# Performance work log

Hardware: AMD Instinct MI355X
Metric: run time of the kernel (lower is better)

## Reference

```python
import jax, jax.numpy as jnp
import numpy as np

N = 50000      # nodes
E = 800000     # edges
H = 128        # hidden_features
DEPTH = 5
G = 64         # graphs in batch
EPS = 1e-5


def _ln(x, g, b):
    m = jnp.mean(x, axis=-1, keepdims=True)
    v = jnp.mean((x - m) ** 2, axis=-1, keepdims=True)
    return (x - m) * jax.lax.rsqrt(v + EPS) * g + b


def _lin_init(key, fan_in, fan_out):
    s = 1.0 / np.sqrt(fan_in)
    kw, kb = jax.random.split(key)
    return (jax.random.uniform(kw, (fan_in, fan_out), jnp.float32, -s, s),
            jax.random.uniform(kb, (fan_out,), jnp.float32, -s, s))


def setup_inputs() -> dict:
    key = jax.random.key(0)
    ks = jax.random.split(key, 16)
    inp = {
        'x': jax.random.normal(ks[0], (N, 1), jnp.float32),
        'pos': jax.random.normal(ks[1], (N, 3), jnp.float32),
        'edge_index': jax.random.randint(ks[2], (2, E), 0, N, jnp.int32),
        'cell_offset': jax.random.normal(ks[3], (E, 3), jnp.float32),
        'unit_cell': jax.random.normal(ks[4], (3, 3), jnp.float32),
        'batch_ids': jnp.sort(jax.random.randint(ks[5], (N,), 0, G, jnp.int32)),
    }
    inp['emb_w'], inp['emb_b'] = _lin_init(ks[6], 1, H)
    # stacked per-layer params for lax.scan
    def stack(fn):
        outs = [fn(jax.random.fold_in(ks[7], i)) for i in range(DEPTH)]
        return tuple(jnp.stack(t) for t in zip(*outs))
    def layer_params(k):
        k1, k2, k3, k4 = jax.random.split(k, 4)
        mw1, mb1 = _lin_init(k1, 2 * H + 1, H)
        mw2, mb2 = _lin_init(k2, H, H)
        uw1, ub1 = _lin_init(k3, 2 * H, H)
        uw2, ub2 = _lin_init(k4, H, H)
        ones = jnp.ones((H,), jnp.float32); zeros = jnp.zeros((H,), jnp.float32)
        return (mw1, mb1, ones, zeros, mw2, mb2, ones, zeros,
                uw1, ub1, ones, zeros, uw2, ub2, ones, zeros)
    (inp['msg_w1'], inp['msg_b1'], inp['msg_g1'], inp['msg_be1'],
     inp['msg_w2'], inp['msg_b2'], inp['msg_g2'], inp['msg_be2'],
     inp['upd_w1'], inp['upd_b1'], inp['upd_g1'], inp['upd_be1'],
     inp['upd_w2'], inp['upd_b2'], inp['upd_g2'], inp['upd_be2']) = stack(layer_params)
    inp['pred_w1'], inp['pred_b1'] = _lin_init(ks[8], H, H)
    inp['pred_w2'], inp['pred_b2'] = _lin_init(ks[9], H, 1)
    return inp


def reference(x, pos, edge_index, cell_offset, unit_cell, batch_ids,
              emb_w, emb_b,
              msg_w1, msg_b1, msg_g1, msg_be1, msg_w2, msg_b2, msg_g2, msg_be2,
              upd_w1, upd_b1, upd_g1, upd_be1, upd_w2, upd_b2, upd_g2, upd_be2,
              pred_w1, pred_b1, pred_w2, pred_b2):
    src, dst = edge_index[0], edge_index[1]  # PyG: x_j = source, x_i = target
    h = x @ emb_w + emb_b  # [N, H]
    # PBC distances
    corrected = pos[dst] - cell_offset @ unit_cell  # [E, 3]
    dist = jnp.linalg.norm(corrected - pos[src], axis=-1, keepdims=True)  # [E, 1]

    def step(h, p):
        (mw1, mb1, mg1, mbe1, mw2, mb2, mg2, mbe2,
         uw1, ub1, ug1, ube1, uw2, ub2, ug2, ube2) = p
        msg = jnp.concatenate([h[dst], h[src], dist], axis=-1)  # [E, 2H+1]
        msg = jax.nn.relu(_ln(msg @ mw1 + mb1, mg1, mbe1))
        msg = jax.nn.relu(_ln(msg @ mw2 + mb2, mg2, mbe2))
        aggr = jax.ops.segment_sum(msg, dst, num_segments=N)  # scatter-add to targets
        u = jnp.concatenate([h, aggr], axis=-1)  # [N, 2H]
        u = jax.nn.relu(_ln(u @ uw1 + ub1, ug1, ube1))
        u = jax.nn.relu(_ln(u @ uw2 + ub2, ug2, ube2))
        return h + u, None  # residual

    params = (msg_w1, msg_b1, msg_g1, msg_be1, msg_w2, msg_b2, msg_g2, msg_be2,
              upd_w1, upd_b1, upd_g1, upd_be1, upd_w2, upd_b2, upd_g2, upd_be2)
    h, _ = jax.lax.scan(step, h, params)
    pooled = jax.ops.segment_sum(h, batch_ids, num_segments=G)  # global_add_pool
    return jax.nn.relu(pooled @ pred_w1 + pred_b1) @ pred_w2 + pred_b2  # [G, 1]
```

## Files before the change

kernel.cpp:

```cpp
#include <hip/hip_runtime.h>
#include <hip/hip_bf16.h>

#define NN 50000
#define NE 800000
#define HD 128
#define DEPTH 5
#define NG 64
#define LNEPS 1e-5f

typedef __attribute__((ext_vector_type(8))) short bf8;
typedef __attribute__((ext_vector_type(4))) float f4;

static __device__ __forceinline__ unsigned short bf1(float x) {
    __hip_bfloat16 b = __float2bfloat16(x);
    unsigned short r;
    __builtin_memcpy(&r, &b, 2);
    return r;
}
static __device__ __forceinline__ unsigned int cvt2(float a, float b) {
    float2 t; t.x = a; t.y = b;
    __hip_bfloat162 h = __float22bfloat162_rn(t);
    unsigned int r;
    __builtin_memcpy(&r, &h, 4);
    return r;
}

__global__ void pack_weights(const float* __restrict__ msg_w1, const float* __restrict__ msg_w2,
                             const float* __restrict__ upd_w1, const float* __restrict__ upd_w2,
                             unsigned short* __restrict__ packed) {
    const int which = blockIdx.y & 3, layer = blockIdx.y >> 2;
    const int t = blockIdx.x * 256 + threadIdx.x;
    const float* src; int K; unsigned short* dst;
    unsigned short* lbase = packed + layer * 98304;
    if (which == 0)      { src = msg_w1 + layer*257*HD; K = 256; dst = lbase; }
    else if (which == 1) { src = msg_w2 + layer*HD*HD;  K = 128; dst = lbase + 32768; }
    else if (which == 2) { src = upd_w1 + layer*256*HD; K = 256; dst = lbase + 49152; }
    else                 { src = upd_w2 + layer*HD*HD;  K = 128; dst = lbase + 81920; }
    if (t >= K * HD) return;
    const int e = t & 7, l = (t >> 3) & 63, f = (t >> 9) & 7, s = t >> 12;
    const int kk = s*32 + ((l >> 4) << 3) + e;
    const int k = (which & 1) ? ((kk & 7)*16 + (kk >> 3)) : kk;
    const int n = f*16 + (l & 15);
    dst[t] = bf1(src[k*HD + n]);
}

__global__ void embed_kernel(const float* __restrict__ x, const float* __restrict__ emb_w,
                             const float* __restrict__ emb_b,
                             float* __restrict__ h, unsigned short* __restrict__ hb) {
    const int i = blockIdx.x * 256 + threadIdx.x;
    const int n = i >> 7, j = i & 127;
    const float v = x[n] * emb_w[j] + emb_b[j];
    h[i] = v; hb[i] = bf1(v);
}

__global__ void hist_kernel(const int* __restrict__ ei, int* __restrict__ cnt) {
    const int e = blockIdx.x * 256 + threadIdx.x;
    atomicAdd(&cnt[ei[NE + e]], 1);
}

__global__ __launch_bounds__(1024) void scan_kernel(const int* __restrict__ cnt,
                                                    int* __restrict__ cur) {
    __shared__ int part[1024];
    const int t = threadIdx.x;
    const int per = 49;
    const int base = t * per;
    int s = 0;
    for (int i = 0; i < per; ++i) { const int idx = base + i; if (idx < NN) s += cnt[idx]; }
    part[t] = s; __syncthreads();
    for (int st = 1; st < 1024; st <<= 1) {
        const int v = (t >= st) ? part[t - st] : 0;
        __syncthreads();
        part[t] += v;
        __syncthreads();
    }
    int run = (t == 0) ? 0 : part[t - 1];
    for (int i = 0; i < per; ++i) {
        const int idx = base + i;
        if (idx < NN) { cur[idx] = run; run += cnt[idx]; }
    }
}

__global__ void scatter_kernel(const int* __restrict__ ei, int* __restrict__ cur,
                               int* __restrict__ sidx, int* __restrict__ ssrc,
                               int* __restrict__ sdst) {
    const int e = blockIdx.x * 256 + threadIdx.x;
    const int d = ei[NE + e];
    const int p = atomicAdd(&cur[d], 1);
    sidx[p] = e; ssrc[p] = ei[e]; sdst[p] = d;
}

__global__ void dist_kernel(const float* __restrict__ pos, const int* __restrict__ sidx,
                            const int* __restrict__ ssrc, const int* __restrict__ sdst,
                            const float* __restrict__ cell, const float* __restrict__ U,
                            float* __restrict__ dist) {
    const int p = blockIdx.x * 256 + threadIdx.x;
    const int e = sidx[p];
    const int s = ssrc[p], d = sdst[p];
    const float c0 = cell[e*3], c1 = cell[e*3+1], c2 = cell[e*3+2];
    const float ox = c0*U[0] + c1*U[3] + c2*U[6];
    const float oy = c0*U[1] + c1*U[4] + c2*U[7];
    const float oz = c0*U[2] + c1*U[5] + c2*U[8];
    const float dx = pos[d*3]   - ox - pos[s*3];
    const float dy = pos[d*3+1] - oy - pos[s*3+1];
    const float dz = pos[d*3+2] - oz - pos[s*3+2];
    dist[p] = sqrtf(dx*dx + dy*dy + dz*dz);
}

__global__ __launch_bounds__(128, 4) void edge_kernel(
    const unsigned short* __restrict__ hb, const float* __restrict__ dist,
    const int* __restrict__ ssrc, const int* __restrict__ sdst,
    const unsigned short* __restrict__ pw,
    const float* __restrict__ w1last, const float* __restrict__ b1,
    const float* __restrict__ g1, const float* __restrict__ be1,
    const float* __restrict__ b2, const float* __restrict__ g2,
    const float* __restrict__ be2, float* __restrict__ aggr)
{
    __shared__ unsigned short lds[64 * 128];
    __shared__ int dstl[64];
    char* ldsb = (char*)lds;
    const int tid = threadIdx.x, blk = blockIdx.x;
    const int l = tid & 63, wv = tid >> 6;
    const int li = l & 15, gq = l >> 4;

    if (tid < 64) dstl[tid] = sdst[blk*64 + tid];

    const int rowA = wv*32 + li, rowB = rowA + 16;
    const int eA = blk*64 + rowA, eB = blk*64 + rowB;
    const unsigned short* pDA = hb + sdst[eA]*HD + gq*8;
    const unsigned short* pSA = hb + ssrc[eA]*HD + gq*8;
    const unsigned short* pDB = hb + sdst[eB]*HD + gq*8;
    const unsigned short* pSB = hb + ssrc[eB]*HD + gq*8;

    f4 acc[2][8];
    #pragma unroll
    for (int m = 0; m < 2; ++m)
        #pragma unroll
        for (int f = 0; f < 8; ++f) { f4 z = {0.f,0.f,0.f,0.f}; acc[m][f] = z; }

    #pragma unroll
    for (int s = 0; s < 8; ++s) {
        bf8 breg[8];
        #pragma unroll
        for (int f = 0; f < 8; ++f) breg[f] = *(const bf8*)(pw + s*4096 + f*512 + l*8);
        const bf8 aA = (s < 4) ? *(const bf8*)(pDA + s*32) : *(const bf8*)(pSA + (s-4)*32);
        const bf8 aB = (s < 4) ? *(const bf8*)(pDB + s*32) : *(const bf8*)(pSB + (s-4)*32);
        #pragma unroll
        for (int f = 0; f < 8; ++f) {
            acc[0][f] = __builtin_amdgcn_mfma_f32_16x16x32_bf16(aA, breg[f], acc[0][f], 0, 0, 0);
            acc[1][f] = __builtin_amdgcn_mfma_f32_16x16x32_bf16(aB, breg[f], acc[1][f], 0, 0, 0);
        }
    }

    {
        float bb[8], wl[8], gg[8], be[8];
        #pragma unroll
        for (int f = 0; f < 8; ++f) {
            const int n = f*16 + li;
            bb[f] = b1[n]; wl[f] = w1last[n]; gg[f] = g1[n]; be[f] = be1[n];
        }
        #pragma unroll
        for (int m = 0; m < 2; ++m) {
            const float4 d4 = *(const float4*)(dist + blk*64 + wv*32 + m*16 + gq*4);
            const float dsv[4] = {d4.x, d4.y, d4.z, d4.w};
            float ps[4] = {0,0,0,0}, pq[4] = {0,0,0,0};
            #pragma unroll
            for (int f = 0; f < 8; ++f)
                #pragma unroll
                for (int r = 0; r < 4; ++r) {
                    const float v = acc[m][f][r] + bb[f] + dsv[r]*wl[f];
                    acc[m][f][r] = v;
                    ps[r] += v; pq[r] += v*v;
                }
            #pragma unroll
            for (int mm = 1; mm < 16; mm <<= 1)
                #pragma unroll
                for (int r = 0; r < 4; ++r) {
                    ps[r] += __shfl_xor(ps[r], mm);
                    pq[r] += __shfl_xor(pq[r], mm);
                }
            #pragma unroll
            for (int r = 0; r < 4; ++r) {
                const float mean = ps[r] * (1.f/HD);
                const float rstd = rsqrtf(pq[r]*(1.f/HD) - mean*mean + LNEPS);
                const int row = wv*32 + m*16 + gq*4 + r;
                float vv[8];
                #pragma unroll
                for (int f = 0; f < 8; ++f)
                    vv[f] = fmaxf((acc[m][f][r] - mean)*rstd*gg[f] + be[f], 0.f);
                uint4 u;
                u.x = cvt2(vv[0], vv[1]); u.y = cvt2(vv[2], vv[3]);
                u.z = cvt2(vv[4], vv[5]); u.w = cvt2(vv[6], vv[7]);
                *(uint4*)(ldsb + ((row*256 + li*16) ^ ((row & 7) << 4))) = u;
            }
        }
    }

    const unsigned short* pw2 = pw + 32768;
    f4 acc2[2][8];
    #pragma unroll
    for (int m = 0; m < 2; ++m)
        #pragma unroll
        for (int f = 0; f < 8; ++f) { f4 z = {0.f,0.f,0.f,0.f}; acc2[m][f] = z; }
    #pragma unroll
    for (int s = 0; s < 4; ++s) {
        bf8 breg[8];
        #pragma unroll
        for (int f = 0; f < 8; ++f) breg[f] = *(const bf8*)(pw2 + s*4096 + f*512 + l*8);
        #pragma unroll
        for (int m = 0; m < 2; ++m) {
            const int ar = wv*32 + m*16 + li;
            const bf8 a = *(const bf8*)(ldsb + ((ar*256 + s*64 + gq*16) ^ ((ar & 7) << 4)));
            #pragma unroll
            for (int f = 0; f < 8; ++f)
                acc2[m][f] = __builtin_amdgcn_mfma_f32_16x16x32_bf16(a, breg[f], acc2[m][f], 0, 0, 0);
        }
    }

    {
        float bb2[8], gg2[8], be2v[8];
        #pragma unroll
        for (int f = 0; f < 8; ++f) {
            const int n = f*16 + li;
            bb2[f] = b2[n]; gg2[f] = g2[n]; be2v[f] = be2[n];
        }
        #pragma unroll
        for (int m = 0; m < 2; ++m) {
            float ps[4] = {0,0,0,0}, pq[4] = {0,0,0,0};
            #pragma unroll
            for (int f = 0; f < 8; ++f)
                #pragma unroll
                for (int r = 0; r < 4; ++r) {
                    const float v = acc2[m][f][r] + bb2[f];
                    acc2[m][f][r] = v;
                    ps[r] += v; pq[r] += v*v;
                }
            #pragma unroll
            for (int mm = 1; mm < 16; mm <<= 1)
                #pragma unroll
                for (int r = 0; r < 4; ++r) {
                    ps[r] += __shfl_xor(ps[r], mm);
                    pq[r] += __shfl_xor(pq[r], mm);
                }
            #pragma unroll
            for (int r = 0; r < 4; ++r) {
                const float mean = ps[r] * (1.f/HD);
                const float rstd = rsqrtf(pq[r]*(1.f/HD) - mean*mean + LNEPS);
                const int row = wv*32 + m*16 + gq*4 + r;
                float vv[8];
                #pragma unroll
                for (int f = 0; f < 8; ++f)
                    vv[f] = fmaxf((acc2[m][f][r] - mean)*rstd*gg2[f] + be2v[f], 0.f);
                uint4 u;
                u.x = cvt2(vv[0], vv[1]); u.y = cvt2(vv[2], vv[3]);
                u.z = cvt2(vv[4], vv[5]); u.w = cvt2(vv[6], vv[7]);
                *(uint4*)(ldsb + ((row*256 + li*16) ^ ((row & 7) << 4))) = u;
            }
        }
    }
    __syncthreads();

    {
        const int j = tid;
        const int jj = (j & 7)*16 + (j >> 3);
        int curd = dstl[0];
        float a0 = 0.f;
        #pragma unroll 4
        for (int row = 0; row < 64; ++row) {
            const int d = dstl[row];
            const unsigned short u = *(const unsigned short*)(ldsb + ((row*256 + j*2) ^ ((row & 7) << 4)));
            const float v = __uint_as_float(((unsigned int)u) << 16);
            if (d != curd) { unsafeAtomicAdd(&aggr[curd*HD + jj], a0); a0 = 0.f; curd = d; }
            a0 += v;
        }
        unsafeAtomicAdd(&aggr[curd*HD + jj], a0);
    }
}

__global__ __launch_bounds__(128, 4) void node_kernel(
    unsigned short* __restrict__ hb, float* __restrict__ aggr,
    const unsigned short* __restrict__ pw,
    const float* __restrict__ b1, const float* __restrict__ g1, const float* __restrict__ be1,
    const float* __restrict__ b2, const float* __restrict__ g2, const float* __restrict__ be2,
    float* __restrict__ h)
{
    __shared__ unsigned short lds[64 * 128];
    char* ldsb = (char*)lds;
    const int tid = threadIdx.x, blk = blockIdx.x;
    const int l = tid & 63, wv = tid >> 6;
    const int li = l & 15, gq = l >> 4;

    const int rowA = wv*32 + li, rowB = rowA + 16;
    const int nA = blk*64 + rowA, nB = blk*64 + rowB;
    const int ncA = (nA < NN) ? nA : NN - 1;
    const int ncB = (nB < NN) ? nB : NN - 1;
    const unsigned short* pHA = hb + ncA*HD + gq*8;
    const unsigned short* pHB = hb + ncB*HD + gq*8;
    float* pAA = aggr + ncA*HD + gq*8;
    float* pAB = aggr + ncB*HD + gq*8;

    f4 acc[2][8];
    #pragma unroll
    for (int m = 0; m < 2; ++m)
        #pragma unroll
        for (int f = 0; f < 8; ++f) { f4 z = {0.f,0.f,0.f,0.f}; acc[m][f] = z; }

    #pragma unroll
    for (int s = 0; s < 8; ++s) {
        bf8 breg[8];
        #pragma unroll
        for (int f = 0; f < 8; ++f) breg[f] = *(const bf8*)(pw + s*4096 + f*512 + l*8);
        bf8 aA, aB;
        if (s < 4) {
            aA = *(const bf8*)(pHA + s*32);
            aB = *(const bf8*)(pHB + s*32);
        } else {
            const float4 a0 = *(const float4*)(pAA + (s-4)*32);
            const float4 a1 = *(const float4*)(pAA + (s-4)*32 + 4);
            const float4 c0 = *(const float4*)(pAB + (s-4)*32);
            const float4 c1 = *(const float4*)(pAB + (s-4)*32 + 4);
            union { unsigned int u[4]; bf8 v; } pk;
            pk.u[0] = cvt2(a0.x, a0.y); pk.u[1] = cvt2(a0.z, a0.w);
            pk.u[2] = cvt2(a1.x, a1.y); pk.u[3] = cvt2(a1.z, a1.w);
            aA = pk.v;
            pk.u[0] = cvt2(c0.x, c0.y); pk.u[1] = cvt2(c0.z, c0.w);
            pk.u[2] = cvt2(c1.x, c1.y); pk.u[3] = cvt2(c1.z, c1.w);
            aB = pk.v;
        }
        #pragma unroll
        for (int f = 0; f < 8; ++f) {
            acc[0][f] = __builtin_amdgcn_mfma_f32_16x16x32_bf16(aA, breg[f], acc[0][f], 0, 0, 0);
            acc[1][f] = __builtin_amdgcn_mfma_f32_16x16x32_bf16(aB, breg[f], acc[1][f], 0, 0, 0);
        }
    }

    {
        const float4 z = {0.f,0.f,0.f,0.f};
        #pragma unroll
        for (int s = 0; s < 4; ++s) {
            if (nA < NN) { *(float4*)(pAA + s*32) = z; *(float4*)(pAA + s*32 + 4) = z; }
            if (nB < NN) { *(float4*)(pAB + s*32) = z; *(float4*)(pAB + s*32 + 4) = z; }
        }
    }

    {
        float bb[8], gg[8], be[8];
        #pragma unroll
        for (int f = 0; f < 8; ++f) {
            const int n = f*16 + li;
            bb[f] = b1[n]; gg[f] = g1[n]; be[f] = be1[n];
        }
        #pragma unroll
        for (int m = 0; m < 2; ++m) {
            float ps[4] = {0,0,0,0}, pq[4] = {0,0,0,0};
            #pragma unroll
            for (int f = 0; f < 8; ++f)
                #pragma unroll
                for (int r = 0; r < 4; ++r) {
                    const float v = acc[m][f][r] + bb[f];
                    acc[m][f][r] = v;
                    ps[r] += v; pq[r] += v*v;
                }
            #pragma unroll
            for (int mm = 1; mm < 16; mm <<= 1)
                #pragma unroll
                for (int r = 0; r < 4; ++r) {
                    ps[r] += __shfl_xor(ps[r], mm);
                    pq[r] += __shfl_xor(pq[r], mm);
                }
            #pragma unroll
            for (int r = 0; r < 4; ++r) {
                const float mean = ps[r] * (1.f/HD);
                const float rstd = rsqrtf(pq[r]*(1.f/HD) - mean*mean + LNEPS);
                const int row = wv*32 + m*16 + gq*4 + r;
                float vv[8];
                #pragma unroll
                for (int f = 0; f < 8; ++f)
                    vv[f] = fmaxf((acc[m][f][r] - mean)*rstd*gg[f] + be[f], 0.f);
                uint4 u;
                u.x = cvt2(vv[0], vv[1]); u.y = cvt2(vv[2], vv[3]);
                u.z = cvt2(vv[4], vv[5]); u.w = cvt2(vv[6], vv[7]);
                *(uint4*)(ldsb + ((row*256 + li*16) ^ ((row & 7) << 4))) = u;
            }
        }
    }

    const unsigned short* pw2 = pw + 32768;
    f4 acc2[2][8];
    #pragma unroll
    for (int m = 0; m < 2; ++m)
        #pragma unroll
        for (int f = 0; f < 8; ++f) { f4 z = {0.f,0.f,0.f,0.f}; acc2[m][f] = z; }
    #pragma unroll
    for (int s = 0; s < 4; ++s) {
        bf8 breg[8];
        #pragma unroll
        for (int f = 0; f < 8; ++f) breg[f] = *(const bf8*)(pw2 + s*4096 + f*512 + l*8);
        #pragma unroll
        for (int m = 0; m < 2; ++m) {
            const int ar = wv*32 + m*16 + li;
            const bf8 a = *(const bf8*)(ldsb + ((ar*256 + s*64 + gq*16) ^ ((ar & 7) << 4)));
            #pragma unroll
            for (int f = 0; f < 8; ++f)
                acc2[m][f] = __builtin_amdgcn_mfma_f32_16x16x32_bf16(a, breg[f], acc2[m][f], 0, 0, 0);
        }
    }

    {
        float bb2[8], gg2[8], be2v[8];
        #pragma unroll
        for (int f = 0; f < 8; ++f) {
            const int n = f*16 + li;
            bb2[f] = b2[n]; gg2[f] = g2[n]; be2v[f] = be2[n];
        }
        #pragma unroll
        for (int m = 0; m < 2; ++m) {
            float ps[4] = {0,0,0,0}, pq[4] = {0,0,0,0};
            #pragma unroll
            for (int f = 0; f < 8; ++f)
                #pragma unroll
                for (int r = 0; r < 4; ++r) {
                    const float v = acc2[m][f][r] + bb2[f];
                    acc2[m][f][r] = v;
                    ps[r] += v; pq[r] += v*v;
                }
            #pragma unroll
            for (int mm = 1; mm < 16; mm <<= 1)
                #pragma unroll
                for (int r = 0; r < 4; ++r) {
                    ps[r] += __shfl_xor(ps[r], mm);
                    pq[r] += __shfl_xor(pq[r], mm);
                }
            #pragma unroll
            for (int r = 0; r < 4; ++r) {
                const int node = blk*64 + wv*32 + m*16 + gq*4 + r;
                if (node < NN) {
                    const float mean = ps[r] * (1.f/HD);
                    const float rstd = rsqrtf(pq[r]*(1.f/HD) - mean*mean + LNEPS);
                    #pragma unroll
                    for (int f = 0; f < 8; ++f) {
                        const int n = f*16 + li;
                        float v = (acc2[m][f][r] - mean)*rstd*gg2[f] + be2v[f];
                        v = fmaxf(v, 0.f);
                        const int idx = node*HD + n;
                        const float nh = h[idx] + v;
                        h[idx] = nh;
                        hb[idx] = bf1(nh);
                    }
                }
            }
        }
    }
}

__global__ void pool_kernel(const float* __restrict__ h, const int* __restrict__ bids,
                            float* __restrict__ pooled) {
    const int j = threadIdx.x;
    const int n0 = blockIdx.x * 256;
    if (n0 >= NN) return;
    int cur = bids[n0];
    float acc = 0.f;
    for (int i = 0; i < 256; ++i) {
        const int n = n0 + i;
        if (n >= NN) break;
        const int b = bids[n];
        if (b != cur) { unsafeAtomicAdd(&pooled[cur*HD + j], acc); acc = 0.f; cur = b; }
        acc += h[n*HD + j];
    }
    unsafeAtomicAdd(&pooled[cur*HD + j], acc);
}

__global__ void pred_kernel(const float* __restrict__ pooled, const float* __restrict__ w1,
                            const float* __restrict__ pb1, const float* __restrict__ w2,
                            const float* __restrict__ pb2, float* __restrict__ out) {
    const int g = blockIdx.x, j = threadIdx.x;
    __shared__ float pg[128];
    __shared__ float red[128];
    pg[j] = pooled[g*HD + j];
    __syncthreads();
    float z = pb1[j];
    for (int k = 0; k < 128; ++k) z += pg[k] * w1[k*HD + j];
    red[j] = fmaxf(z, 0.f) * w2[j];
    __syncthreads();
    for (int st = 64; st > 0; st >>= 1) {
        if (j < st) red[j] += red[j + st];
        __syncthreads();
    }
    if (j == 0) out[g] = red[0] + pb2[0];
}

extern "C" void kernel_launch(void* const* d_in, const int* in_sizes, int n_in,
                              void* d_out, int out_size, void* d_ws, size_t ws_size,
                              hipStream_t stream) {
    const float* x       = (const float*)d_in[0];
    const float* pos     = (const float*)d_in[1];
    const int*   ei      = (const int*)  d_in[2];
    const float* cell    = (const float*)d_in[3];
    const float* U       = (const float*)d_in[4];
    const int*   bids    = (const int*)  d_in[5];
    const float* emb_w   = (const float*)d_in[6];
    const float* emb_b   = (const float*)d_in[7];
    const float* msg_w1  = (const float*)d_in[8];
    const float* msg_b1  = (const float*)d_in[9];
    const float* msg_g1  = (const float*)d_in[10];
    const float* msg_be1 = (const float*)d_in[11];
    const float* msg_w2  = (const float*)d_in[12];
    const float* msg_b2  = (const float*)d_in[13];
    const float* msg_g2  = (const float*)d_in[14];
    const float* msg_be2 = (const float*)d_in[15];
    const float* upd_w1  = (const float*)d_in[16];
    const float* upd_b1  = (const float*)d_in[17];
    const float* upd_g1  = (const float*)d_in[18];
    const float* upd_be1 = (const float*)d_in[19];
    const float* upd_w2  = (const float*)d_in[20];
    const float* upd_b2  = (const float*)d_in[21];
    const float* upd_g2  = (const float*)d_in[22];
    const float* upd_be2 = (const float*)d_in[23];
    const float* pred_w1 = (const float*)d_in[24];
    const float* pred_b1 = (const float*)d_in[25];
    const float* pred_w2 = (const float*)d_in[26];
    const float* pred_b2 = (const float*)d_in[27];

    char* ws = (char*)d_ws;
    float*          h      = (float*)          ws;
    unsigned short* hb     = (unsigned short*)(ws + 25600000);
    float*          aggr   = (float*)         (ws + 38400000);
    float*          dist   = (float*)         (ws + 64000000);
    float*          pooled = (float*)         (ws + 67200000);
    unsigned short* packed = (unsigned short*)(ws + 67232768);
    int*            cnt    = (int*)           (ws + 68215808);
    int*            cur    = (int*)           (ws + 68416512);
    int*            sidx   = (int*)           (ws + 68617216);
    int*            ssrc   = (int*)           (ws + 71817216);
    int*            sdst   = (int*)           (ws + 75017216);

    hipMemsetAsync(aggr, 0, (size_t)NN * HD * sizeof(float), stream);
    hipMemsetAsync(pooled, 0, (size_t)NG * HD * sizeof(float), stream);
    hipMemsetAsync(cnt, 0, (size_t)NN * sizeof(int), stream);

    dim3 pgrid(128, DEPTH * 4);
    pack_weights<<<pgrid, 256, 0, stream>>>(msg_w1, msg_w2, upd_w1, upd_w2, packed);
    embed_kernel<<<(NN * HD) / 256, 256, 0, stream>>>(x, emb_w, emb_b, h, hb);

    hist_kernel<<<NE / 256, 256, 0, stream>>>(ei, cnt);
    scan_kernel<<<1, 1024, 0, stream>>>(cnt, cur);
    scatter_kernel<<<NE / 256, 256, 0, stream>>>(ei, cur, sidx, ssrc, sdst);
    dist_kernel<<<NE / 256, 256, 0, stream>>>(pos, sidx, ssrc, sdst, cell, U, dist);

    for (int layer = 0; layer < DEPTH; ++layer) {
        const unsigned short* pl = packed + layer * 98304;
        edge_kernel<<<NE / 64, 128, 0, stream>>>(
            hb, dist, ssrc, sdst, pl,
            msg_w1 + layer*257*HD + 256*HD,
            msg_b1 + layer*HD, msg_g1 + layer*HD, msg_be1 + layer*HD,
            msg_b2 + layer*HD, msg_g2 + layer*HD, msg_be2 + layer*HD,
            aggr);
        node_kernel<<<(NN + 63) / 64, 128, 0, stream>>>(
            hb, aggr, pl + 49152,
            upd_b1 + layer*HD, upd_g1 + layer*HD, upd_be1 + layer*HD,
            upd_b2 + layer*HD, upd_g2 + layer*HD, upd_be2 + layer*HD,
            h);
    }

    pool_kernel<<<(NN + 255) / 256, 128, 0, stream>>>(h, bids, pooled);
    pred_kernel<<<NG, 128, 0, stream>>>(pooled, pred_w1, pred_b1, pred_w2, pred_b2, (float*)d_out);
}
```

Baseline: 1.414 ms.

## Precompute per-node first message-layer projections and gather them per edge

The first message linear layer is split by linearity: h@W_dst (plus bias) and h@W_src are computed once per node in a new y_kernel. The edge kernel then gathers and adds the two projected rows plus the distance term instead of running a K=256 MFMA GEMM per edge. This cuts the first-layer GEMM work from per-edge to per-node, at the cost of an extra kernel, a 256-wide bf16 y buffer, and an extra bf16 rounding of the pre-LayerNorm sums. Per-edge gathers stay the same size (two 128-wide bf16 rows).

```diff
diff --git a/kernel.cpp b/kernel.cpp
--- a/kernel.cpp
+++ b/kernel.cpp
@@ -25,15 +25,25 @@
     return r;
 }
 
+
 __global__ void pack_weights(const float* __restrict__ msg_w1, const float* __restrict__ msg_w2,
                              const float* __restrict__ upd_w1, const float* __restrict__ upd_w2,
                              unsigned short* __restrict__ packed) {
     const int which = blockIdx.y & 3, layer = blockIdx.y >> 2;
     const int t = blockIdx.x * 256 + threadIdx.x;
+    unsigned short* lbase = packed + layer * 98304;
+    if (which == 0) {
+        if (t >= 32768) return;
+        const int e = t & 7, l = (t >> 3) & 63, f = (t >> 9) & 15, s = t >> 13;
+        const int k = s*32 + ((l >> 4) << 3) + e;
+        const float* W = msg_w1 + layer*257*HD;
+        const float v = (f < 8) ? W[k*HD + f*16 + (l & 15)]
+                                : W[(k + 128)*HD + (f - 8)*16 + (l & 15)];
+        lbase[t] = bf1(v);
+        return;
+    }
     const float* src; int K; unsigned short* dst;
-    unsigned short* lbase = packed + layer * 98304;
-    if (which == 0)      { src = msg_w1 + layer*257*HD; K = 256; dst = lbase; }
-    else if (which == 1) { src = msg_w2 + layer*HD*HD;  K = 128; dst = lbase + 32768; }
+    if (which == 1)      { src = msg_w2 + layer*HD*HD;  K = 128; dst = lbase + 32768; }
     else if (which == 2) { src = upd_w1 + layer*256*HD; K = 256; dst = lbase + 49152; }
     else                 { src = upd_w2 + layer*HD*HD;  K = 128; dst = lbase + 81920; }
     if (t >= K * HD) return;
@@ -42,6 +52,19 @@
     const int k = (which & 1) ? ((kk & 7)*16 + (kk >> 3)) : kk;
     const int n = f*16 + (l & 15);
     dst[t] = bf1(src[k*HD + n]);
+}
+
+__global__ void pack_sig(const float* __restrict__ msg_w1, const float* __restrict__ msg_g1,
+                         const float* __restrict__ msg_be1, float* __restrict__ sig) {
+    const int t = blockIdx.x * 256 + threadIdx.x;
+    if (t >= DEPTH * 384) return;
+    const int layer = t / 384, w3 = (t % 384) / 128, i = t % 128;
+    const int col = (i & 7)*16 + (i >> 3);
+    float v;
+    if (w3 == 0)      v = msg_w1[layer*257*HD + 256*HD + col];
+    else if (w3 == 1) v = msg_g1[layer*HD + col];
+    else              v = msg_be1[layer*HD + col];
+    sig[t] = v;
 }
 
 __global__ void embed_kernel(const float* __restrict__ x, const float* __restrict__ emb_w,
@@ -106,12 +129,67 @@
     dist[p] = sqrtf(dx*dx + dy*dy + dz*dz);
 }
 
+__global__ void y_kernel(const unsigned short* __restrict__ hb,
+                         const unsigned short* __restrict__ pw,
+                         const float* __restrict__ b1, unsigned short* __restrict__ y) {
+    const int tid = threadIdx.x, blk = blockIdx.x;
+    const int l = tid & 63, wv = tid >> 6;
+    const int li = l & 15, gq = l >> 4;
+    const int rowA = wv*32 + li, rowB = rowA + 16;
+    const int nA = blk*64 + rowA, nB = blk*64 + rowB;
+    const int ncA = (nA < NN) ? nA : NN - 1;
+    const int ncB = (nB < NN) ? nB : NN - 1;
+    const unsigned short* pHA = hb + ncA*HD + gq*8;
+    const unsigned short* pHB = hb + ncB*HD + gq*8;
+
+    f4 acc[2][16];
+    #pragma unroll
+    for (int m = 0; m < 2; ++m)
+        #pragma unroll
+        for (int f = 0; f < 16; ++f) { f4 z = {0.f,0.f,0.f,0.f}; acc[m][f] = z; }
+
+    #pragma unroll
+    for (int s = 0; s < 4; ++s) {
+        const bf8 aA = *(const bf8*)(pHA + s*32);
+        const bf8 aB = *(const bf8*)(pHB + s*32);
+        #pragma unroll
+        for (int f = 0; f < 16; ++f) {
+            const bf8 b = *(const bf8*)(pw + s*8192 + f*512 + l*8);
+            acc[0][f] = __builtin_amdgcn_mfma_f32_16x16x32_bf16(aA, b, acc[0][f], 0, 0, 0);
+            acc[1][f] = __builtin_amdgcn_mfma_f32_16x16x32_bf16(aB, b, acc[1][f], 0, 0, 0);
+        }
+    }
+
+    float bv[8];
+    #pragma unroll
+    for (int f = 0; f < 8; ++f) bv[f] = b1[f*16 + li];
+
+    #pragma unroll
+    for (int m = 0; m < 2; ++m)
+        #pragma unroll
+        for (int r = 0; r < 4; ++r) {
+            const int node = blk*64 + wv*32 + m*16 + gq*4 + r;
+            if (node < NN) {
+                uint4 u;
+                u.x = cvt2(acc[m][0][r]+bv[0], acc[m][1][r]+bv[1]);
+                u.y = cvt2(acc[m][2][r]+bv[2], acc[m][3][r]+bv[3]);
+                u.z = cvt2(acc[m][4][r]+bv[4], acc[m][5][r]+bv[5]);
+                u.w = cvt2(acc[m][6][r]+bv[6], acc[m][7][r]+bv[7]);
+                *(uint4*)(y + node*256 + li*8) = u;
+                uint4 v;
+                v.x = cvt2(acc[m][8][r],  acc[m][9][r]);
+                v.y = cvt2(acc[m][10][r], acc[m][11][r]);
+                v.z = cvt2(acc[m][12][r], acc[m][13][r]);
+                v.w = cvt2(acc[m][14][r], acc[m][15][r]);
+                *(uint4*)(y + node*256 + 128 + li*8) = v;
+            }
+        }
+}
+
 __global__ __launch_bounds__(128, 4) void edge_kernel(
-    const unsigned short* __restrict__ hb, const float* __restrict__ dist,
+    const unsigned short* __restrict__ y, const float* __restrict__ dist,
     const int* __restrict__ ssrc, const int* __restrict__ sdst,
-    const unsigned short* __restrict__ pw,
-    const float* __restrict__ w1last, const float* __restrict__ b1,
-    const float* __restrict__ g1, const float* __restrict__ be1,
+    const unsigned short* __restrict__ pw2, const float* __restrict__ sig,
     const float* __restrict__ b2, const float* __restrict__ g2,
     const float* __restrict__ be2, float* __restrict__ aggr)
 {
@@ -124,78 +202,67 @@
 
     if (tid < 64) dstl[tid] = sdst[blk*64 + tid];
 
-    const int rowA = wv*32 + li, rowB = rowA + 16;
-    const int eA = blk*64 + rowA, eB = blk*64 + rowB;
-    const unsigned short* pDA = hb + sdst[eA]*HD + gq*8;
-    const unsigned short* pSA = hb + ssrc[eA]*HD + gq*8;
-    const unsigned short* pDB = hb + sdst[eB]*HD + gq*8;
-    const unsigned short* pSB = hb + ssrc[eB]*HD + gq*8;
-
-    f4 acc[2][8];
-    #pragma unroll
-    for (int m = 0; m < 2; ++m)
-        #pragma unroll
-        for (int f = 0; f < 8; ++f) { f4 z = {0.f,0.f,0.f,0.f}; acc[m][f] = z; }
-
-    #pragma unroll
-    for (int s = 0; s < 8; ++s) {
-        bf8 breg[8];
-        #pragma unroll
-        for (int f = 0; f < 8; ++f) breg[f] = *(const bf8*)(pw + s*4096 + f*512 + l*8);
-        const bf8 aA = (s < 4) ? *(const bf8*)(pDA + s*32) : *(const bf8*)(pSA + (s-4)*32);
-        const bf8 aB = (s < 4) ? *(const bf8*)(pDB + s*32) : *(const bf8*)(pSB + (s-4)*32);
-        #pragma unroll
-        for (int f = 0; f < 8; ++f) {
-            acc[0][f] = __builtin_amdgcn_mfma_f32_16x16x32_bf16(aA, breg[f], acc[0][f], 0, 0, 0);
-            acc[1][f] = __builtin_amdgcn_mfma_f32_16x16x32_bf16(aB, breg[f], acc[1][f], 0, 0, 0);
-        }
-    }
-
     {
-        float bb[8], wl[8], gg[8], be[8];
-        #pragma unroll
-        for (int f = 0; f < 8; ++f) {
-            const int n = f*16 + li;
-            bb[f] = b1[n]; wl[f] = w1last[n]; gg[f] = g1[n]; be[f] = be1[n];
-        }
-        #pragma unroll
-        for (int m = 0; m < 2; ++m) {
-            const float4 d4 = *(const float4*)(dist + blk*64 + wv*32 + m*16 + gq*4);
-            const float dsv[4] = {d4.x, d4.y, d4.z, d4.w};
-            float ps[4] = {0,0,0,0}, pq[4] = {0,0,0,0};
-            #pragma unroll
-            for (int f = 0; f < 8; ++f)
-                #pragma unroll
-                for (int r = 0; r < 4; ++r) {
-                    const float v = acc[m][f][r] + bb[f] + dsv[r]*wl[f];
-                    acc[m][f][r] = v;
-                    ps[r] += v; pq[r] += v*v;
-                }
-            #pragma unroll
-            for (int mm = 1; mm < 16; mm <<= 1)
-                #pragma unroll
-                for (int r = 0; r < 4; ++r) {
-                    ps[r] += __shfl_xor(ps[r], mm);
-                    pq[r] += __shfl_xor(pq[r], mm);
-                }
-            #pragma unroll
-            for (int r = 0; r < 4; ++r) {
-                const float mean = ps[r] * (1.f/HD);
-                const float rstd = rsqrtf(pq[r]*(1.f/HD) - mean*mean + LNEPS);
-                const int row = wv*32 + m*16 + gq*4 + r;
-                float vv[8];
-                #pragma unroll
-                for (int f = 0; f < 8; ++f)
-                    vv[f] = fmaxf((acc[m][f][r] - mean)*rstd*gg[f] + be[f], 0.f);
-                uint4 u;
-                u.x = cvt2(vv[0], vv[1]); u.y = cvt2(vv[2], vv[3]);
-                u.z = cvt2(vv[4], vv[5]); u.w = cvt2(vv[6], vv[7]);
-                *(uint4*)(ldsb + ((row*256 + li*16) ^ ((row & 7) << 4))) = u;
+        const int rl = l >> 1, half = l & 1;
+        const int row = wv*32 + rl;
+        const int e = blk*64 + row;
+        const int dn = sdst[e], sn = ssrc[e];
+        const float dv = dist[e];
+        const unsigned short* pd = y + dn*256 + half*64;
+        const unsigned short* pS = y + sn*256 + 128 + half*64;
+        const float* wl = sig + half*64;
+
+        float msum[64];
+        #pragma unroll
+        for (int c = 0; c < 8; ++c) {
+            const uint4 ud = *(const uint4*)(pd + c*8);
+            const uint4 us = *(const uint4*)(pS + c*8);
+            const float4 wa = *(const float4*)(wl + c*8);
+            const float4 wb = *(const float4*)(wl + c*8 + 4);
+            const unsigned int du[4] = {ud.x, ud.y, ud.z, ud.w};
+            const unsigned int su[4] = {us.x, us.y, us.z, us.w};
+            const float ww[8] = {wa.x,wa.y,wa.z,wa.w, wb.x,wb.y,wb.z,wb.w};
+            #pragma unroll
+            for (int k = 0; k < 4; ++k) {
+                const float d0 = __uint_as_float(du[k] << 16);
+                const float d1 = __uint_as_float(du[k] & 0xffff0000u);
+                const float s0 = __uint_as_float(su[k] << 16);
+                const float s1 = __uint_as_float(su[k] & 0xffff0000u);
+                msum[c*8 + 2*k]     = d0 + s0 + dv*ww[2*k];
+                msum[c*8 + 2*k + 1] = d1 + s1 + dv*ww[2*k+1];
             }
         }
-    }
-
-    const unsigned short* pw2 = pw + 32768;
+        float s1 = 0.f, s2 = 0.f;
+        #pragma unroll
+        for (int i = 0; i < 64; ++i) { s1 += msum[i]; s2 += msum[i]*msum[i]; }
+        s1 += __shfl_xor(s1, 1);
+        s2 += __shfl_xor(s2, 1);
+        const float mean = s1 * (1.f/HD);
+        const float rstd = rsqrtf(s2*(1.f/HD) - mean*mean + LNEPS);
+
+        const float* g1p = sig + 128 + half*64;
+        const float* e1p = sig + 256 + half*64;
+        const int rsw = (row & 7) << 4;
+        const int base = row*256 + half*128;
+        #pragma unroll
+        for (int c = 0; c < 8; ++c) {
+            const float4 ga = *(const float4*)(g1p + c*8);
+            const float4 gb = *(const float4*)(g1p + c*8 + 4);
+            const float4 ea = *(const float4*)(e1p + c*8);
+            const float4 eb = *(const float4*)(e1p + c*8 + 4);
+            const float gg[8] = {ga.x,ga.y,ga.z,ga.w, gb.x,gb.y,gb.z,gb.w};
+            const float ee[8] = {ea.x,ea.y,ea.z,ea.w, eb.x,eb.y,eb.z,eb.w};
+            float t[8];
+            #pragma unroll
+            for (int k = 0; k < 8; ++k)
+                t[k] = fmaxf((msum[c*8+k] - mean)*rstd*gg[k] + ee[k], 0.f);
+            uint4 u;
+            u.x = cvt2(t[0], t[1]); u.y = cvt2(t[2], t[3]);
+            u.z = cvt2(t[4], t[5]); u.w = cvt2(t[6], t[7]);
+            *(uint4*)(ldsb + ((base + c*16) ^ rsw)) = u;
+        }
+    }
+
     f4 acc2[2][8];
     #pragma unroll
     for (int m = 0; m < 2; ++m)
@@ -532,6 +599,8 @@
     int*            sidx   = (int*)           (ws + 68617216);
     int*            ssrc   = (int*)           (ws + 71817216);
     int*            sdst   = (int*)           (ws + 75017216);
+    float*          sig    = (float*)         (ws + 78217216);
+    unsigned short* y      = (unsigned short*)(ws + 78224896);
 
     hipMemsetAsync(aggr, 0, (size_t)NN * HD * sizeof(float), stream);
     hipMemsetAsync(pooled, 0, (size_t)NG * HD * sizeof(float), stream);
@@ -539,6 +608,7 @@
 
     dim3 pgrid(128, DEPTH * 4);
     pack_weights<<<pgrid, 256, 0, stream>>>(msg_w1, msg_w2, upd_w1, upd_w2, packed);
+    pack_sig<<<(DEPTH*384 + 255)/256, 256, 0, stream>>>(msg_w1, msg_g1, msg_be1, sig);
     embed_kernel<<<(NN * HD) / 256, 256, 0, stream>>>(x, emb_w, emb_b, h, hb);
 
     hist_kernel<<<NE / 256, 256, 0, stream>>>(ei, cnt);
@@ -548,10 +618,9 @@
 
     for (int layer = 0; layer < DEPTH; ++layer) {
         const unsigned short* pl = packed + layer * 98304;
+        y_kernel<<<(NN + 63) / 64, 128, 0, stream>>>(hb, pl, msg_b1 + layer*HD, y);
         edge_kernel<<<NE / 64, 128, 0, stream>>>(
-            hb, dist, ssrc, sdst, pl,
-            msg_w1 + layer*257*HD + 256*HD,
-            msg_b1 + layer*HD, msg_g1 + layer*HD, msg_be1 + layer*HD,
+            y, dist, ssrc, sdst, pl + 32768, sig + layer*384,
             msg_b2 + layer*HD, msg_g2 + layer*HD, msg_be2 + layer*HD,
             aggr);
         node_kernel<<<(NN + 63) / 64, 128, 0, stream>>>(
```

New measurement: 1.494 ms. 1.06x slower.
